# Performance work log

Measured on AMD Instinct MI355X. Metric: run time of the kernel, lower is better.

The kernel has to match this reference:

```python
import jax, jax.numpy as jnp
import numpy as np

LN_EPS = 1e-6

def _log_g(x):
    return jnp.where(x >= 0, jnp.log(jax.nn.relu(x) + 0.5), -jax.nn.softplus(-x))

def setup_inputs() -> dict:
    key = jax.random.key(0)
    k1, k2 = jax.random.split(key)
    B, T, D = 8, 4096, 1024
    x = jax.random.normal(k1, (B, T, D), dtype=jnp.float32)
    W = jax.random.normal(k2, (D, 2 * D), dtype=jnp.float32) * (1.0 / np.sqrt(D))
    b = jnp.zeros((2 * D,), dtype=jnp.float32)
    gamma = jnp.ones((D,), dtype=jnp.float32)
    beta = jnp.zeros((D,), dtype=jnp.float32)
    return {"x": x, "W": W, "b": b, "gamma": gamma, "beta": beta}

def reference(x, W, b, gamma, beta):
    # projection: [B,T,D] @ [D,2D] -> [B,T,2D]
    projected = jnp.einsum('btd,de->bte', x, W) + b
    h_tilde, k = jnp.split(projected, 2, axis=-1)
    log_coeffs = -jax.nn.softplus(k)          # log(1-z)
    log_z = -jax.nn.softplus(-k)               # log(z)
    log_values = log_z + _log_g(h_tilde)
    # parallel scan in log space along time axis (-2)
    a_star = jnp.cumsum(log_coeffs, axis=-2)
    log_h0_plus_b_star = jax.lax.associative_scan(jnp.logaddexp, log_values - a_star, axis=-2)
    h = jnp.exp(a_star + log_h0_plus_b_star)
    # residual + LayerNorm (eps = flax nnx default 1e-6)
    y = x + h
    mu = jnp.mean(y, axis=-1, keepdims=True)
    var = jnp.mean(jnp.square(y - mu), axis=-1, keepdims=True)
    return (y - mu) * jax.lax.rsqrt(var + LN_EPS) * gamma + beta
```

## Files before the change

### kernel.cpp

```cpp
#include <hip/hip_runtime.h>
#include <hip/hip_bf16.h>

#define B_  8
#define T_  4096
#define D_  1024
#define M_  (B_*T_)
#define N_  (2*D_)
#define K_  D_
#define NC_ 32
#define C_  (T_/NC_)

typedef short bf16x8 __attribute__((ext_vector_type(8)));
typedef float f32x4  __attribute__((ext_vector_type(4)));

__device__ __forceinline__ unsigned short f2bf(float f) {
  union { float f; unsigned int u; } v; v.f = f;
  unsigned int r = (v.u + 0x7fffu + ((v.u >> 16) & 1u)) >> 16;
  return (unsigned short)r;
}

__device__ __forceinline__ float bf2f(unsigned short u) {
  union { unsigned int u; float f; } v; v.u = ((unsigned int)u) << 16; return v.f;
}

__device__ __forceinline__ float bflo(unsigned int u) {
  union { unsigned int u; float f; } v; v.u = u << 16; return v.f;
}
__device__ __forceinline__ float bfhi(unsigned int u) {
  union { unsigned int u; float f; } v; v.u = u & 0xffff0000u; return v.f;
}

__device__ __forceinline__ float sigm(float x) {
  return 1.0f / (1.0f + __expf(-x));
}

__device__ __forceinline__ void async16(const void* g, void* l) {
  __builtin_amdgcn_global_load_lds((const __attribute__((address_space(1))) void*)g,
                                   (__attribute__((address_space(3))) void*)l,
                                   16, 0, 0);
}

__global__ void cast_x_kernel(const float* __restrict__ x, unsigned short* __restrict__ xb) {
  const long n4 = (long)M_ * K_ / 4;
  long i = (long)blockIdx.x * blockDim.x + threadIdx.x;
  const long stride = (long)gridDim.x * blockDim.x;
  for (; i < n4; i += stride) {
    float4 v = ((const float4*)x)[i];
    ushort4 o;
    o.x = f2bf(v.x); o.y = f2bf(v.y); o.z = f2bf(v.z); o.w = f2bf(v.w);
    ((ushort4*)xb)[i] = o;
  }
}

__global__ void cast_wt_kernel(const float* __restrict__ W, unsigned short* __restrict__ Wt) {
  __shared__ float tile[32][33];
  const int n0 = blockIdx.x * 32, k0 = blockIdx.y * 32;
  const int tx = threadIdx.x, ty = threadIdx.y;
  for (int i = 0; i < 32; i += 8)
    tile[ty + i][tx] = W[(size_t)(k0 + ty + i) * N_ + n0 + tx];
  __syncthreads();
  for (int i = 0; i < 32; i += 8)
    Wt[(size_t)(n0 + ty + i) * K_ + k0 + tx] = f2bf(tile[tx][ty + i]);
}

#define BM 256
#define BN 256
#define BK 64
#define LDSA(b) ((b)*32768)
#define LDSB(b) ((b)*32768 + 16384)

#define BARX()  __builtin_amdgcn_s_barrier()
#define LGKM0() asm volatile("s_waitcnt lgkmcnt(0)" ::: "memory")
#define LGKM8() asm volatile("s_waitcnt lgkmcnt(8)" ::: "memory")
#define SB0()   __builtin_amdgcn_sched_barrier(0)
#define VM8()   asm volatile("s_waitcnt vmcnt(8)" ::: "memory")
#define VM0()   asm volatile("s_waitcnt vmcnt(0)" ::: "memory")

#define STAGE_Bt(BUF, KOFF) do {                                                \
    _Pragma("unroll")                                                           \
    for (int r = 0; r < 4; ++r)                                                 \
      async16(aB + (KOFF) + r*64*K_, lds + LDSB(BUF) + w*512 + r*4096);         \
  } while (0)
#define STAGE_At(BUF, KOFF) do {                                                \
    _Pragma("unroll")                                                           \
    for (int r = 0; r < 4; ++r)                                                 \
      async16(aA + (KOFF) + r*64*K_, lds + LDSA(BUF) + w*512 + r*4096);         \
  } while (0)

#define RD_A(MBASE, BUF) do {                                                   \
    _Pragma("unroll")                                                           \
    for (int m = 0; m < 4; ++m) {                                               \
      af[m][0] = *(const bf16x8*)(lds + LDSA(BUF) + (rowA + (MBASE + m)*16)*64 + cc0); \
      af[m][1] = *(const bf16x8*)(lds + LDSA(BUF) + (rowA + (MBASE + m)*16)*64 + cc1); \
    } } while (0)
#define RD_B(NBASE, BUF) do {                                                   \
    _Pragma("unroll")                                                           \
    for (int n = 0; n < 2; ++n) {                                               \
      bfr[NBASE + n][0] = *(const bf16x8*)(lds + LDSB(BUF) + (rowB + (NBASE + n)*16)*64 + cc0); \
      bfr[NBASE + n][1] = *(const bf16x8*)(lds + LDSB(BUF) + (rowB + (NBASE + n)*16)*64 + cc1); \
    } } while (0)

#define MFMA_Q(MB, NB) do {                                                     \
    __builtin_amdgcn_s_setprio(1);                                              \
    _Pragma("unroll")                                                           \
    for (int m = 0; m < 4; ++m)                                                 \
      _Pragma("unroll")                                                         \
      for (int n = 0; n < 2; ++n) {                                             \
        acc[MB+m][NB+n] = __builtin_amdgcn_mfma_f32_16x16x32_bf16(af[m][0], bfr[NB+n][0], acc[MB+m][NB+n], 0, 0, 0); \
        acc[MB+m][NB+n] = __builtin_amdgcn_mfma_f32_16x16x32_bf16(af[m][1], bfr[NB+n][1], acc[MB+m][NB+n], 0, 0, 0); \
      }                                                                         \
    __builtin_amdgcn_s_setprio(0);                                              \
  } while (0)

#define TILE(BUF, DO_STAGE, KOFF, VMW) do {                                     \
                                                                        \
    RD_A(0, BUF); RD_B(0, BUF);                                                 \
    LGKM8();                                                                    \
    BARX(); LGKM0(); SB0();                                                     \
    MFMA_Q(0, 0);                                                               \
    BARX();                                                                     \
                                                                        \
    RD_B(2, BUF);                                                               \
    BARX(); LGKM0(); SB0();                                                     \
    MFMA_Q(0, 2);                                                               \
    BARX();                                                                     \
                                                                        \
    if (DO_STAGE) STAGE_Bt(BUF, KOFF);                                          \
    RD_A(4, BUF);                                                               \
    BARX(); LGKM0(); SB0();                                                     \
    MFMA_Q(4, 0);                                                               \
    BARX();                                                                     \
                                                                        \
    if (DO_STAGE) STAGE_At(BUF, KOFF);                                          \
    MFMA_Q(4, 2);                                                               \
    VMW;                                                                        \
    BARX();                                                                     \
  } while (0)

__global__ __launch_bounds__(512, 2) void gemm_kernel(
    const unsigned short* __restrict__ A,
    const unsigned short* __restrict__ Bt,
    const float* __restrict__ bias,
    unsigned short* __restrict__ Sout,
    unsigned short* __restrict__ Gout) {
  __shared__ unsigned short lds[65536];

  const int tid  = threadIdx.x;
  const int w    = tid >> 6;
  const int lane = tid & 63;
  const int wm   = w >> 2;
  const int wn   = w & 3;
  const int quad = lane >> 4, n15 = lane & 15;

  const int bid   = blockIdx.x;
  const int xcd   = bid & 7;
  const int j     = bid >> 3;
  const int n_idx = j & 7;
  const int m_idx = (j >> 3) * 8 + xcd;
  const int m0 = m_idx * BM, n0 = n_idx * BN;

  const int lr = lane >> 3, lg = lane & 7;
  const int sg8 = (lg ^ lr) * 8;
  const unsigned short* aA = A  + (size_t)(m0 + w*8 + lr) * K_ + sg8;
  const unsigned short* aB = Bt + (size_t)(n0 + w*8 + lr) * K_ + sg8;

  const int n7  = n15 & 7;
  const int cc0 = (quad ^ n7) * 8;
  const int cc1 = cc0 ^ 32;
  const int rowA = wm * 128 + n15;
  const int rowB = wn * 64  + n15;

  f32x4 acc[8][4];
  #pragma unroll
  for (int i = 0; i < 8; ++i)
    #pragma unroll
    for (int jj = 0; jj < 4; ++jj) acc[i][jj] = (f32x4){0.f, 0.f, 0.f, 0.f};

  bf16x8 af[4][2], bfr[4][2];

  STAGE_Bt(0, 0);  STAGE_At(0, 0);
  STAGE_Bt(1, 64); STAGE_At(1, 64);
  VM8();
  BARX();

  int koff = 128;
  #pragma unroll 1
  for (int it = 0; it < 7; ++it) {
    TILE(0, 1, koff,      VM8());
    TILE(1, 1, koff + 64, VM8());
    koff += 128;
  }
  TILE(0, 0, 0, VM0());
  TILE(1, 0, 0, ((void)0));

  const bool is_k = (n0 >= D_);
  unsigned short* __restrict__ dst = is_k ? Sout : Gout;
  const int d0 = is_k ? (n0 - D_) : n0;
  float bv[4];
  #pragma unroll
  for (int jj = 0; jj < 4; ++jj) bv[jj] = bias[n0 + wn*64 + jj*16 + n15];

  #pragma unroll
  for (int i = 0; i < 8; ++i) {
    #pragma unroll
    for (int jj = 0; jj < 4; ++jj) {
      const int col = wn*64 + jj*16 + n15;
      #pragma unroll
      for (int r = 0; r < 4; ++r) {
        const int row = wm*128 + i*16 + quad*4 + r;
        const float val = acc[i][jj][r] + bv[jj];
        const float o = is_k ? sigm(val)
                             : ((val >= 0.0f) ? (val + 0.5f) : sigm(val));
        const int slot = (col >> 3) ^ (row & 7);
        lds[row*256 + slot*8 + (col & 7)] = f2bf(o);
      }
    }
  }
  __syncthreads();
  const int trow = tid >> 5;
  const int cg   = tid & 31;
  #pragma unroll
  for (int rr = 0; rr < 16; ++rr) {
    const int row = rr*16 + trow;
    const uint4 v = *(const uint4*)(lds + row*256 + ((cg ^ (row & 7)) * 8));
    *(uint4*)(dst + (size_t)(m0 + row) * D_ + d0 + cg*8) = v;
  }
}

__global__ void chunk_agg_kernel(const unsigned short* __restrict__ S,
                                 const unsigned short* __restrict__ G,
                                 float* __restrict__ AggA, float* __restrict__ AggV) {
  const int p = blockIdx.x * 256 + threadIdx.x;
  const int d = p * 2;
  const int c = blockIdx.y;
  const int b = blockIdx.z;
  size_t base2 = ((((size_t)b * T_ + (size_t)c * C_) * D_) + d) >> 1;
  const unsigned int* __restrict__ S2 = (const unsigned int*)S;
  const unsigned int* __restrict__ G2 = (const unsigned int*)G;
  float Aa0 = 1.0f, V0 = 0.0f, Aa1 = 1.0f, V1 = 0.0f;
  for (int t = 0; t < C_; ++t) {
    const unsigned int sv = S2[base2];
    const unsigned int gv = G2[base2];
    const float s0 = bflo(sv), s1 = bfhi(sv);
    const float g0 = bflo(gv), g1 = bfhi(gv);
    const float a0 = 1.0f - s0, a1 = 1.0f - s1;
    V0 = fmaf(a0, V0, s0 * g0);
    V1 = fmaf(a1, V1, s1 * g1);
    Aa0 *= a0; Aa1 *= a1;
    base2 += D_ / 2;
  }
  const int idx = (b * NC_ + c) * D_ + d;
  *(float2*)(AggA + idx) = make_float2(Aa0, Aa1);
  *(float2*)(AggV + idx) = make_float2(V0, V1);
}

__global__ void chunk_scan_kernel(const float* __restrict__ AggA, const float* __restrict__ AggV,
                                  float* __restrict__ H0) {
  const int p = blockIdx.x * 256 + threadIdx.x;
  const int d = p * 2;
  const int b = blockIdx.y;
  float h0 = 0.0f, h1 = 0.0f;
  for (int c = 0; c < NC_; ++c) {
    const int idx = (b * NC_ + c) * D_ + d;
    const float2 a = *(const float2*)(AggA + idx);
    const float2 v = *(const float2*)(AggV + idx);
    *(float2*)(H0 + idx) = make_float2(h0, h1);
    h0 = fmaf(a.x, h0, v.x);
    h1 = fmaf(a.y, h1, v.y);
  }
}

__global__ __launch_bounds__(1024, 1) void scan_ln_kernel(
    const unsigned short* __restrict__ S, const unsigned short* __restrict__ G,
    const float* __restrict__ x, const float* __restrict__ H0,
    const float* __restrict__ gamma, const float* __restrict__ beta,
    float* __restrict__ out) {
  __shared__ float yb[16 * 1024];
  const int d = threadIdx.x;
  const int c = blockIdx.x;
  const int b = blockIdx.y;
  const int wid = d >> 6, lane = d & 63;

  float h = H0[(b * NC_ + c) * D_ + d];
  float2 gam2[8], bet2[8];
  for (int j = 0; j < 8; ++j) {
    gam2[j] = *(const float2*)(gamma + lane * 2 + 128 * j);
    bet2[j] = *(const float2*)(beta  + lane * 2 + 128 * j);
  }

  size_t base = ((size_t)b * T_ + (size_t)c * C_) * D_ + d;
  for (int batch = 0; batch < 8; ++batch) {
    for (int tt = 0; tt < 16; ++tt) {
      const size_t idx = base + (size_t)tt * D_;
      const float s = bf2f(S[idx]);
      const float g = bf2f(G[idx]);
      h = fmaf(s, g - h, h);
      yb[tt * 1024 + d] = x[idx] + h;
    }
    __syncthreads();
    {
      float sy = 0.0f, sq = 0.0f;
      float2 yv[8];
      for (int j = 0; j < 8; ++j) {
        const float2 v = *(const float2*)(&yb[wid * 1024 + lane * 2 + 128 * j]);
        yv[j] = v;
        sy += v.x + v.y;
        sq += v.x * v.x + v.y * v.y;
      }
      for (int o = 32; o > 0; o >>= 1) {
        sy += __shfl_down(sy, o);
        sq += __shfl_down(sq, o);
      }
      sy = __shfl(sy, 0); sq = __shfl(sq, 0);
      const float mu   = sy * (1.0f / D_);
      const float rstd = rsqrtf(sq * (1.0f / D_) - mu * mu + 1e-6f);
      const size_t obase = ((size_t)b * T_ + (size_t)c * C_ + (size_t)batch * 16 + wid) * D_;
      for (int j = 0; j < 8; ++j) {
        float2 o2;
        o2.x = (yv[j].x - mu) * rstd * gam2[j].x + bet2[j].x;
        o2.y = (yv[j].y - mu) * rstd * gam2[j].y + bet2[j].y;
        *(float2*)(out + obase + lane * 2 + 128 * j) = o2;
      }
    }
    __syncthreads();
    base += (size_t)16 * D_;
  }
}

extern "C" void kernel_launch(void* const* d_in, const int* in_sizes, int n_in,
                              void* d_out, int out_size, void* d_ws, size_t ws_size,
                              hipStream_t stream) {
  const float* x     = (const float*)d_in[0];
  const float* W     = (const float*)d_in[1];
  const float* bias  = (const float*)d_in[2];
  const float* gamma = (const float*)d_in[3];
  const float* beta  = (const float*)d_in[4];
  float* out = (float*)d_out;

  char* ws = (char*)d_ws;
  unsigned short* Wt = (unsigned short*)ws;  ws += (size_t)N_ * K_ * 2;
  unsigned short* Xb = (unsigned short*)ws;  ws += (size_t)M_ * K_ * 2;
  unsigned short* S  = (unsigned short*)ws;  ws += (size_t)M_ * D_ * 2;
  unsigned short* G  = (unsigned short*)ws;  ws += (size_t)M_ * D_ * 2;
  float* AggA = (float*)ws;                  ws += (size_t)B_ * NC_ * D_ * 4;
  float* AggV = (float*)ws;                  ws += (size_t)B_ * NC_ * D_ * 4;
  float* H0   = (float*)ws;                  ws += (size_t)B_ * NC_ * D_ * 4;

  cast_x_kernel<<<4096, 256, 0, stream>>>(x, Xb);
  cast_wt_kernel<<<dim3(N_ / 32, K_ / 32), dim3(32, 8), 0, stream>>>(W, Wt);
  gemm_kernel<<<1024, 512, 0, stream>>>(Xb, Wt, bias, S, G);
  chunk_agg_kernel<<<dim3(D_ / 512, NC_, B_), 256, 0, stream>>>(S, G, AggA, AggV);
  chunk_scan_kernel<<<dim3(D_ / 512, B_), 256, 0, stream>>>(AggA, AggV, H0);
  scan_ln_kernel<<<dim3(NC_, B_), 1024, 0, stream>>>(S, G, x, H0, gamma, beta, out);
}
```

Baseline: 482.0 us.

## Fuse fp32-to-bf16 cast of x into GEMM A-tile staging

Drops the separate cast_x kernel and its bf16 workspace copy of x. The GEMM now loads fp32 rows of x into registers, converts them to bf16, and writes them into the swizzled LDS A buffer. It replaces the asynchronous global-to-LDS A loads with synchronous register loads. This saves a full read and write pass over x. In exchange, each n-block reads twice as many A bytes, register pressure rises in an already register-heavy kernel, and the compiler-inserted waits for the register loads may stall the pipeline.

```diff
diff --git a/kernel.cpp b/kernel.cpp
--- a/kernel.cpp
+++ b/kernel.cpp
@@ -38,18 +38,6 @@
   __builtin_amdgcn_global_load_lds((const __attribute__((address_space(1))) void*)g,
                                    (__attribute__((address_space(3))) void*)l,
                                    16, 0, 0);
-}
-
-__global__ void cast_x_kernel(const float* __restrict__ x, unsigned short* __restrict__ xb) {
-  const long n4 = (long)M_ * K_ / 4;
-  long i = (long)blockIdx.x * blockDim.x + threadIdx.x;
-  const long stride = (long)gridDim.x * blockDim.x;
-  for (; i < n4; i += stride) {
-    float4 v = ((const float4*)x)[i];
-    ushort4 o;
-    o.x = f2bf(v.x); o.y = f2bf(v.y); o.z = f2bf(v.z); o.w = f2bf(v.w);
-    ((ushort4*)xb)[i] = o;
-  }
 }
 
 __global__ void cast_wt_kernel(const float* __restrict__ W, unsigned short* __restrict__ Wt) {
@@ -81,11 +69,23 @@
     for (int r = 0; r < 4; ++r)                                                 \
       async16(aB + (KOFF) + r*64*K_, lds + LDSB(BUF) + w*512 + r*4096);         \
   } while (0)
-#define STAGE_At(BUF, KOFF) do {                                                \
-    _Pragma("unroll")                                                           \
-    for (int r = 0; r < 4; ++r)                                                 \
-      async16(aA + (KOFF) + r*64*K_, lds + LDSA(BUF) + w*512 + r*4096);         \
-  } while (0)
+
+#define STAGE_A_LOAD(KOFF) do {                                                 \
+    _Pragma("unroll")                                                           \
+    for (int r = 0; r < 4; ++r) {                                               \
+      av0[r] = *(const float4*)(aAx + (KOFF) + r*64*K_);                        \
+      av1[r] = *(const float4*)(aAx + (KOFF) + r*64*K_ + 4);                    \
+    } } while (0)
+#define STAGE_A_WRITE(BUF) do {                                                 \
+    _Pragma("unroll")                                                           \
+    for (int r = 0; r < 4; ++r) {                                               \
+      bf16x8 pk;                                                                \
+      pk[0] = (short)f2bf(av0[r].x); pk[1] = (short)f2bf(av0[r].y);             \
+      pk[2] = (short)f2bf(av0[r].z); pk[3] = (short)f2bf(av0[r].w);             \
+      pk[4] = (short)f2bf(av1[r].x); pk[5] = (short)f2bf(av1[r].y);             \
+      pk[6] = (short)f2bf(av1[r].z); pk[7] = (short)f2bf(av1[r].w);             \
+      *(bf16x8*)(lds + LDSA(BUF) + r*4096 + w*512 + lane*8) = pk;               \
+    } } while (0)
 
 #define RD_A(MBASE, BUF) do {                                                   \
     _Pragma("unroll")                                                           \
@@ -120,6 +120,7 @@
     MFMA_Q(0, 0);                                                               \
     BARX();                                                                     \
                                                                         \
+    if (DO_STAGE) STAGE_A_LOAD(KOFF);                                           \
     RD_B(2, BUF);                                                               \
     BARX(); LGKM0(); SB0();                                                     \
     MFMA_Q(0, 2);                                                               \
@@ -131,14 +132,14 @@
     MFMA_Q(4, 0);                                                               \
     BARX();                                                                     \
                                                                         \
-    if (DO_STAGE) STAGE_At(BUF, KOFF);                                          \
+    if (DO_STAGE) STAGE_A_WRITE(BUF);                                           \
     MFMA_Q(4, 2);                                                               \
     VMW;                                                                        \
     BARX();                                                                     \
   } while (0)
 
 __global__ __launch_bounds__(512, 2) void gemm_kernel(
-    const unsigned short* __restrict__ A,
+    const float* __restrict__ X,
     const unsigned short* __restrict__ Bt,
     const float* __restrict__ bias,
     unsigned short* __restrict__ Sout,
@@ -161,8 +162,8 @@
 
   const int lr = lane >> 3, lg = lane & 7;
   const int sg8 = (lg ^ lr) * 8;
-  const unsigned short* aA = A  + (size_t)(m0 + w*8 + lr) * K_ + sg8;
-  const unsigned short* aB = Bt + (size_t)(n0 + w*8 + lr) * K_ + sg8;
+  const float*          aAx = X  + (size_t)(m0 + w*8 + lr) * K_ + sg8;
+  const unsigned short* aB  = Bt + (size_t)(n0 + w*8 + lr) * K_ + sg8;
 
   const int n7  = n15 & 7;
   const int cc0 = (quad ^ n7) * 8;
@@ -177,10 +178,16 @@
     for (int jj = 0; jj < 4; ++jj) acc[i][jj] = (f32x4){0.f, 0.f, 0.f, 0.f};
 
   bf16x8 af[4][2], bfr[4][2];
-
-  STAGE_Bt(0, 0);  STAGE_At(0, 0);
-  STAGE_Bt(1, 64); STAGE_At(1, 64);
-  VM8();
+  float4 av0[4], av1[4];
+
+  STAGE_A_LOAD(0);
+  STAGE_Bt(0, 0);
+  STAGE_Bt(1, 64);
+  STAGE_A_WRITE(0);
+  STAGE_A_LOAD(64);
+  STAGE_A_WRITE(1);
+  LGKM0();
+  VM0();
   BARX();
 
   int koff = 128;
@@ -339,16 +346,14 @@
 
   char* ws = (char*)d_ws;
   unsigned short* Wt = (unsigned short*)ws;  ws += (size_t)N_ * K_ * 2;
-  unsigned short* Xb = (unsigned short*)ws;  ws += (size_t)M_ * K_ * 2;
   unsigned short* S  = (unsigned short*)ws;  ws += (size_t)M_ * D_ * 2;
   unsigned short* G  = (unsigned short*)ws;  ws += (size_t)M_ * D_ * 2;
   float* AggA = (float*)ws;                  ws += (size_t)B_ * NC_ * D_ * 4;
   float* AggV = (float*)ws;                  ws += (size_t)B_ * NC_ * D_ * 4;
   float* H0   = (float*)ws;                  ws += (size_t)B_ * NC_ * D_ * 4;
 
-  cast_x_kernel<<<4096, 256, 0, stream>>>(x, Xb);
   cast_wt_kernel<<<dim3(N_ / 32, K_ / 32), dim3(32, 8), 0, stream>>>(W, Wt);
-  gemm_kernel<<<1024, 512, 0, stream>>>(Xb, Wt, bias, S, G);
+  gemm_kernel<<<1024, 512, 0, stream>>>(x, Wt, bias, S, G);
   chunk_agg_kernel<<<dim3(D_ / 512, NC_, B_), 256, 0, stream>>>(S, G, AggA, AggV);
   chunk_scan_kernel<<<dim3(D_ / 512, B_), 256, 0, stream>>>(AggA, AggV, H0);
   scan_ln_kernel<<<dim3(NC_, B_), 1024, 0, stream>>>(S, G, x, H0, gamma, beta, out);
```

New measurement: 604.8 us. 1.25x slower.
